# Performance work log

Measured on AMD Instinct MI355X. Metric: run time of the kernel, lower is better.

## Reference

```python
import jax, jax.numpy as jnp
import numpy as np

B, L, H, S = 8, 2048, 8, 128


def setup_inputs() -> dict:
    key = jax.random.key(0)
    k1, k2, k3 = jax.random.split(key, 3)
    x = jax.random.normal(k1, (B, L, S), dtype=jnp.float32)
    W = jax.random.normal(k2, (L, H), dtype=jnp.float32)          # per-head Toeplitz logits, W[j, h] fills diagonal -j
    A = jax.random.normal(k3, (H * S, H * S), dtype=jnp.float32)  # bilinear form for stage-2 attention
    return {"x": x, "W": W, "A": A}


def reference(x, W, A):
    Bb, Ll, Ss = x.shape
    Hh = W.shape[1]
    HS = Hh * Ss
    # Stage 1: causal Toeplitz softmax attention per head.
    # Original fills diagonal -j of W_h with W[j, h], masks strictly-upper with -inf, softmaxes rows.
    d = jnp.arange(Ll)[:, None] - jnp.arange(Ll)[None, :]          # (L, L), i - j
    logits = jnp.where(d[..., None] >= 0,
                       W[jnp.clip(d, 0, Ll - 1)],                  # (L, L, H), W[i-j, h] on valid band
                       -jnp.inf)
    P = jax.nn.softmax(logits, axis=1)                             # softmax over key axis j
    attn = jnp.einsum('ijh,bjs->bihs', P, x).reshape(Bb, Ll, HS)   # heads concatenated
    X1 = jnp.concatenate([attn, x], axis=-1)                       # (B, L, (H+1)*S)
    # Stage 2: single-query bilinear attention from last token over previous tokens.
    q = X1[:, -1, :HS]                                             # (B, HS)
    keys = X1[:, :-1, :HS]                                         # (B, L-1, HS)
    scores = jnp.einsum('bd,de,ble->bl', q, A, keys)               # (B, L-1)
    w2 = jax.nn.softmax(scores, axis=-1)
    # values are the raw-x slice X1[:, :-1, HS:] == x[:, :-1, :]
    out = jnp.einsum('bl,bls->bs', w2, x[:, :-1, :])               # (B, S)
    return out
```

## Files before the change

kernel.cpp:

```cpp
#include <hip/hip_runtime.h>

#define L 2048
#define H 8
#define S 128
#define B 8
#define HS 1024

__global__ __launch_bounds__(512) void kA_prep_qpart(const float* __restrict__ W,
                                                     const float* __restrict__ x,
                                                     float* __restrict__ Eb,
                                                     float* __restrict__ Zb,
                                                     float* __restrict__ partial_q,
                                                     unsigned* __restrict__ counters) {
  const int b = blockIdx.x, jc = blockIdx.y;
  const int t = threadIdx.x;
  if (b == 0 && jc == 0 && t < 8) counters[t] = 0u;

  __shared__ float ew[128][H];
  __shared__ float part[16][H][S];
  __shared__ float tot[512];

  const int base = jc * 128;
  const int dhi = L - 1 - base;
#pragma unroll
  for (int k = 0; k < 2; ++k) {
    const int idx = t + k * 512;
    const int i = idx >> 3, h = idx & 7;
    ew[i][h] = expf(W[(size_t)(dhi - i) * H + h]);
  }

  if (jc < H) {
    const int h = jc;
    const int d0 = t * 4;
    float e[4];
    float run = 0.f;
#pragma unroll
    for (int k = 0; k < 4; ++k) {
      float v = expf(W[(size_t)(d0 + k) * H + h]);
      e[k] = v; run += v;
    }
    tot[t] = run;
    __syncthreads();
    for (int off = 1; off < 512; off <<= 1) {
      float v = (t >= off) ? tot[t - off] : 0.f;
      __syncthreads();
      tot[t] += v;
      __syncthreads();
    }
    float c = (t == 0) ? 0.f : tot[t - 1];
    const size_t ebase = (size_t)(b * H + h) * L;
#pragma unroll
    for (int k = 0; k < 4; ++k) {
      c += e[k];
      Eb[ebase + d0 + k] = e[k];
      Zb[ebase + d0 + k] = c;
    }
  }
  __syncthreads();

  const int s4 = t & 31;
  const int r = t >> 5;
  const float4* __restrict__ x4 = (const float4*)(x + (size_t)b * L * S);
  float4 acc[H];
#pragma unroll
  for (int h = 0; h < H; ++h) acc[h] = make_float4(0.f, 0.f, 0.f, 0.f);
#pragma unroll
  for (int k = 0; k < 8; ++k) {
    const int ll = k * 16 + r;
    const int l = base + ll;
    const float4 xv = x4[(size_t)l * 32 + s4];
#pragma unroll
    for (int h = 0; h < H; ++h) {
      const float w = ew[ll][h];
      acc[h].x += w * xv.x; acc[h].y += w * xv.y;
      acc[h].z += w * xv.z; acc[h].w += w * xv.w;
    }
  }
#pragma unroll
  for (int h = 0; h < H; ++h) {
    part[r][h][s4 * 4 + 0] = acc[h].x;
    part[r][h][s4 * 4 + 1] = acc[h].y;
    part[r][h][s4 * 4 + 2] = acc[h].z;
    part[r][h][s4 * 4 + 3] = acc[h].w;
  }
  __syncthreads();
#pragma unroll
  for (int k = 0; k < 2; ++k) {
    const int idx = t + k * 512;
    const int h = idx >> 7, s = idx & 127;
    float sm = 0.f;
#pragma unroll
    for (int rr = 0; rr < 16; ++rr) sm += part[rr][h][s];
    partial_q[((size_t)b * 16 + jc) * HS + idx] = sm;
  }
}

__global__ __launch_bounds__(512) void kB_v(const float* __restrict__ partial_q,
                                            const float* __restrict__ Zb,
                                            const float* __restrict__ A,
                                            float* __restrict__ partial_v) {
  const int ebase = blockIdx.x * 128;
  const int dc = blockIdx.y;
  const int dbase = dc * 64;
  const int t = threadIdx.x;
  __shared__ float ql[8][64];
  __shared__ float p2[4][8][128];
  const float invZ = 1.f / Zb[(size_t)(dc >> 1) * L + (L - 1)];
  {
    const int bb = t >> 6, dl = t & 63;
    const float* __restrict__ pq = partial_q + ((size_t)bb * 16) * HS + dbase + dl;
    float a0 = 0.f, a1 = 0.f, a2 = 0.f, a3 = 0.f;
#pragma unroll
    for (int j4 = 0; j4 < 16; j4 += 4) {
      a0 += pq[(size_t)(j4 + 0) * HS];
      a1 += pq[(size_t)(j4 + 1) * HS];
      a2 += pq[(size_t)(j4 + 2) * HS];
      a3 += pq[(size_t)(j4 + 3) * HS];
    }
    ql[bb][dl] = ((a0 + a1) + (a2 + a3)) * invZ;
  }
  __syncthreads();
  const int el = t & 127, dg = t >> 7;
  const int e = ebase + el;
  const float* __restrict__ Ab = A + (size_t)(dbase + dg * 16) * HS + e;
  float acc[8] = {0.f, 0.f, 0.f, 0.f, 0.f, 0.f, 0.f, 0.f};
#pragma unroll 4
  for (int dd = 0; dd < 16; ++dd) {
    const float a = Ab[(size_t)dd * HS];
    const int d = dg * 16 + dd;
    acc[0] += ql[0][d] * a;
    acc[1] += ql[1][d] * a;
    acc[2] += ql[2][d] * a;
    acc[3] += ql[3][d] * a;
    acc[4] += ql[4][d] * a;
    acc[5] += ql[5][d] * a;
    acc[6] += ql[6][d] * a;
    acc[7] += ql[7][d] * a;
  }
#pragma unroll
  for (int bb = 0; bb < 8; ++bb) p2[dg][bb][el] = acc[bb];
  __syncthreads();
#pragma unroll
  for (int k = 0; k < 2; ++k) {
    const int idx = t + k * 512;
    const int bb = idx >> 7, el2 = idx & 127;
    partial_v[((size_t)bb * 16 + dc) * HS + ebase + el2] =
        (p2[0][bb][el2] + p2[1][bb][el2]) + (p2[2][bb][el2] + p2[3][bb][el2]);
  }
}

__global__ __launch_bounds__(512) void kC_u(const float* __restrict__ x,
                                            const float* __restrict__ partial_v,
                                            float* __restrict__ u_pad) {
  const int b = blockIdx.x, jc = blockIdx.y;
  const int t = threadIdx.x;
  __shared__ float vs[HS];
  __shared__ float up[4][H][128];
#pragma unroll
  for (int k = 0; k < 2; ++k) {
    const int i = t + k * 512;
    float a0 = 0.f, a1 = 0.f, a2 = 0.f, a3 = 0.f;
#pragma unroll
    for (int dcc = 0; dcc < 16; dcc += 4) {
      a0 += partial_v[((size_t)b * 16 + dcc + 0) * HS + i];
      a1 += partial_v[((size_t)b * 16 + dcc + 1) * HS + i];
      a2 += partial_v[((size_t)b * 16 + dcc + 2) * HS + i];
      a3 += partial_v[((size_t)b * 16 + dcc + 3) * HS + i];
    }
    vs[i] = (a0 + a1) + (a2 + a3);
  }
  __syncthreads();
  const int jl = t & 127, sq = t >> 7;
  const int j = jc * 128 + jl;
  const float4* __restrict__ xr = (const float4*)(x + ((size_t)b * L + j) * S) + sq * 8;
  float4 xv[8];
#pragma unroll
  for (int i = 0; i < 8; ++i) xv[i] = xr[i];
  float acc[H];
#pragma unroll
  for (int h = 0; h < H; ++h) {
    const float4* __restrict__ vv = (const float4*)(vs + h * S + sq * 32);
    float a = 0.f;
#pragma unroll
    for (int i = 0; i < 8; ++i) {
      const float4 w = vv[i];
      a += xv[i].x * w.x + xv[i].y * w.y + xv[i].z * w.z + xv[i].w * w.w;
    }
    acc[h] = a;
  }
#pragma unroll
  for (int h = 0; h < H; ++h) up[sq][h][jl] = acc[h];
  __syncthreads();
#pragma unroll
  for (int k = 0; k < 2; ++k) {
    const int idx = t + k * 512;
    const int h = idx >> 7, j2 = idx & 127;
    const float sv = (up[0][h][j2] + up[1][h][j2]) + (up[2][h][j2] + up[3][h][j2]);
    const size_t rowbase = (size_t)(b * H + h) * (2 * L);
    u_pad[rowbase + jc * 128 + j2] = 0.f;
    u_pad[rowbase + L + jc * 128 + j2] = sv;
  }
}

__global__ __launch_bounds__(512) void kDF_out(const float* __restrict__ x,
                                               const float* __restrict__ u_pad,
                                               const float* __restrict__ Eb,
                                               const float* __restrict__ Zb,
                                               float* __restrict__ scores,
                                               unsigned* __restrict__ counters,
                                               float* __restrict__ out) {
  const int b = blockIdx.x, lt = blockIdx.y;
  const int t = threadIdx.x;
  const int tsub = t & 31;
  const int h = (t >> 5) & 7;
  const int dh = t >> 8;
  const int l0 = lt * 128;
  const int Lb = l0 + tsub * 4;

  __shared__ float sred[2][H][128];
  __shared__ float ep[L];
  __shared__ float red[512];
  __shared__ float part[16][S];

  const float* __restrict__ ur = u_pad + (size_t)(b * H + h) * (2 * L) + L;
  const float4* __restrict__ Eh4 = (const float4*)(Eb + (size_t)(b * H + h) * L);
  float acc0 = 0.f, acc1 = 0.f, acc2 = 0.f, acc3 = 0.f;
  for (int chunk = dh; chunk <= lt; chunk += 2) {
    const int dbase = chunk * 128;
    float4 lo = *(const float4*)(ur + Lb - dbase - 4);
    float4 hi = *(const float4*)(ur + Lb - dbase);
#pragma unroll 4
    for (int dd = 0; dd < 128; dd += 4) {
      const int d0 = dbase + dd;
      float4 ev  = Eh4[d0 >> 2];
      float4 nlo = *(const float4*)(ur + Lb - d0 - 8);
      acc0 += ev.x * hi.x; acc1 += ev.x * hi.y; acc2 += ev.x * hi.z; acc3 += ev.x * hi.w;
      acc0 += ev.y * lo.w; acc1 += ev.y * hi.x; acc2 += ev.y * hi.y; acc3 += ev.y * hi.z;
      acc0 += ev.z * lo.z; acc1 += ev.z * lo.w; acc2 += ev.z * hi.x; acc3 += ev.z * hi.y;
      acc0 += ev.w * lo.y; acc1 += ev.w * lo.z; acc2 += ev.w * lo.w; acc3 += ev.w * hi.x;
      hi = lo; lo = nlo;
    }
  }
  const float4 zv = *(const float4*)&Zb[(size_t)(b * H + h) * L + Lb];
  sred[dh][h][tsub * 4 + 0] = acc0 / zv.x;
  sred[dh][h][tsub * 4 + 1] = acc1 / zv.y;
  sred[dh][h][tsub * 4 + 2] = acc2 / zv.z;
  sred[dh][h][tsub * 4 + 3] = acc3 / zv.w;
  __syncthreads();
  if (t < 128) {
    const int l = l0 + t;
    float sc = 0.f;
#pragma unroll
    for (int hh = 0; hh < H; ++hh) sc += sred[0][hh][t] + sred[1][hh][t];
    scores[(size_t)b * L + l] = (l == L - 1) ? -3.4e38f : sc;
  }

  __threadfence();
  __syncthreads();
  __shared__ unsigned lastFlag;
  if (t == 0)
    lastFlag = (atomicAdd(&counters[b], 1u) == 15u) ? 1u : 0u;
  __syncthreads();
  if (!lastFlag) return;

  const int l4 = t * 4;
  const float4 sv4 = *(const float4*)&scores[(size_t)b * L + l4];
  float mx = fmaxf(fmaxf(sv4.x, sv4.y), fmaxf(sv4.z, sv4.w));
  red[t] = mx;
  __syncthreads();
  for (int off = 256; off > 0; off >>= 1) {
    if (t < off) red[t] = fmaxf(red[t], red[t + off]);
    __syncthreads();
  }
  mx = red[0];
  __syncthreads();
  float e0 = expf(sv4.x - mx), e1 = expf(sv4.y - mx);
  float e2 = expf(sv4.z - mx), e3 = expf(sv4.w - mx);
  red[t] = (e0 + e1) + (e2 + e3);
  __syncthreads();
  for (int off = 256; off > 0; off >>= 1) {
    if (t < off) red[t] += red[t + off];
    __syncthreads();
  }
  const float inv = 1.f / red[0];
  ep[l4 + 0] = e0 * inv;
  ep[l4 + 1] = e1 * inv;
  ep[l4 + 2] = e2 * inv;
  ep[l4 + 3] = e3 * inv;
  __syncthreads();

  const int s4 = t & 31;
  const int r = t >> 5;
  const float4* __restrict__ x4 = (const float4*)(x + (size_t)b * L * S);
  float4 acc = make_float4(0.f, 0.f, 0.f, 0.f);
  for (int k = 0; k < 128; ++k) {
    const int l = k * 16 + r;
    const float w = ep[l];
    const float4 xv = x4[(size_t)l * 32 + s4];
    acc.x += w * xv.x; acc.y += w * xv.y; acc.z += w * xv.z; acc.w += w * xv.w;
  }
  part[r][s4 * 4 + 0] = acc.x;
  part[r][s4 * 4 + 1] = acc.y;
  part[r][s4 * 4 + 2] = acc.z;
  part[r][s4 * 4 + 3] = acc.w;
  __syncthreads();
  if (t < S) {
    float smv = 0.f;
#pragma unroll
    for (int rr = 0; rr < 16; ++rr) smv += part[rr][t];
    out[b * S + t] = smv;
  }
}

extern "C" void kernel_launch(void* const* d_in, const int* in_sizes, int n_in,
                              void* d_out, int out_size, void* d_ws, size_t ws_size,
                              hipStream_t stream) {
  const float* x = (const float*)d_in[0];
  const float* W = (const float*)d_in[1];
  const float* A = (const float*)d_in[2];
  float* out = (float*)d_out;

  float* ws        = (float*)d_ws;
  float* Eb        = ws;
  float* Zb        = Eb + (size_t)B * H * L;
  float* partial_q = Zb + (size_t)B * H * L;
  float* partial_v = partial_q + (size_t)B * 16 * HS;
  float* u_pad     = partial_v + (size_t)B * 16 * HS;
  float* scores    = u_pad + (size_t)B * H * 2 * L;
  unsigned* counters = (unsigned*)(scores + (size_t)B * L);

  kA_prep_qpart<<<dim3(B, 16), 512, 0, stream>>>(W, x, Eb, Zb, partial_q, counters);
  kB_v         <<<dim3(8, 16), 512, 0, stream>>>(partial_q, Zb, A, partial_v);
  kC_u         <<<dim3(B, 16), 512, 0, stream>>>(x, partial_v, u_pad);
  kDF_out      <<<dim3(B, 16), 512, 0, stream>>>(x, u_pad, Eb, Zb, scores, counters, out);
}
```

Before: 62.76 us.

## Split triangular Toeplitz convolution in kDF_out into balanced per-chunk blocks

Before, each kDF_out block walked a variable number of 128-wide d-chunks, so work grew with the l-tile and the blocks were unevenly loaded. Now 72 blocks per batch each handle one 256-wide chunk pair of the triangular iteration space and write partial scores. A two-level padded atomic counter picks the last block, which sums the partials before the softmax and weighted sum. This evens out the load and adds parallelism, at the cost of extra partial-score traffic and a more complex completion protocol.

```diff
diff --git a/kernel.cpp b/kernel.cpp
--- a/kernel.cpp
+++ b/kernel.cpp
@@ -14,7 +14,7 @@
                                                      unsigned* __restrict__ counters) {
   const int b = blockIdx.x, jc = blockIdx.y;
   const int t = threadIdx.x;
-  if (b == 0 && jc == 0 && t < 8) counters[t] = 0u;
+  if (b == 0 && jc == 0 && t < 72) counters[t * 16] = 0u;
 
   __shared__ float ew[128][H];
   __shared__ float part[16][H][S];
@@ -206,15 +206,20 @@
                                                const float* __restrict__ u_pad,
                                                const float* __restrict__ Eb,
                                                const float* __restrict__ Zb,
-                                               float* __restrict__ scores,
+                                               float* __restrict__ partial_s,
                                                unsigned* __restrict__ counters,
                                                float* __restrict__ out) {
-  const int b = blockIdx.x, lt = blockIdx.y;
+  const int b = blockIdx.x;
+  const int rr = blockIdx.y;
+  int lt = 0, c = 0;
+  while (c + (lt / 2 + 1) <= rr) { c += lt / 2 + 1; ++lt; }
+  const int dtt = rr - c;
+  const int l0 = lt * 128;
   const int t = threadIdx.x;
   const int tsub = t & 31;
   const int h = (t >> 5) & 7;
   const int dh = t >> 8;
-  const int l0 = lt * 128;
+  const int dbase = dtt * 256 + dh * 128;
   const int Lb = l0 + tsub * 4;
 
   __shared__ float sred[2][H][128];
@@ -222,11 +227,10 @@
   __shared__ float red[512];
   __shared__ float part[16][S];
 
-  const float* __restrict__ ur = u_pad + (size_t)(b * H + h) * (2 * L) + L;
-  const float4* __restrict__ Eh4 = (const float4*)(Eb + (size_t)(b * H + h) * L);
-  float acc0 = 0.f, acc1 = 0.f, acc2 = 0.f, acc3 = 0.f;
-  for (int chunk = dh; chunk <= lt; chunk += 2) {
-    const int dbase = chunk * 128;
+  {
+    const float* __restrict__ ur = u_pad + (size_t)(b * H + h) * (2 * L) + L;
+    const float4* __restrict__ Eh4 = (const float4*)(Eb + (size_t)(b * H + h) * L);
+    float acc0 = 0.f, acc1 = 0.f, acc2 = 0.f, acc3 = 0.f;
     float4 lo = *(const float4*)(ur + Lb - dbase - 4);
     float4 hi = *(const float4*)(ur + Lb - dbase);
 #pragma unroll 4
@@ -240,32 +244,46 @@
       acc0 += ev.w * lo.y; acc1 += ev.w * lo.z; acc2 += ev.w * lo.w; acc3 += ev.w * hi.x;
       hi = lo; lo = nlo;
     }
-  }
-  const float4 zv = *(const float4*)&Zb[(size_t)(b * H + h) * L + Lb];
-  sred[dh][h][tsub * 4 + 0] = acc0 / zv.x;
-  sred[dh][h][tsub * 4 + 1] = acc1 / zv.y;
-  sred[dh][h][tsub * 4 + 2] = acc2 / zv.z;
-  sred[dh][h][tsub * 4 + 3] = acc3 / zv.w;
-  __syncthreads();
-  if (t < 128) {
-    const int l = l0 + t;
-    float sc = 0.f;
-#pragma unroll
-    for (int hh = 0; hh < H; ++hh) sc += sred[0][hh][t] + sred[1][hh][t];
-    scores[(size_t)b * L + l] = (l == L - 1) ? -3.4e38f : sc;
+    const float4 zv = *(const float4*)&Zb[(size_t)(b * H + h) * L + Lb];
+    sred[dh][h][tsub * 4 + 0] = acc0 / zv.x;
+    sred[dh][h][tsub * 4 + 1] = acc1 / zv.y;
+    sred[dh][h][tsub * 4 + 2] = acc2 / zv.z;
+    sred[dh][h][tsub * 4 + 3] = acc3 / zv.w;
+    __syncthreads();
+    if (t < 128) {
+      float sc = 0.f;
+#pragma unroll
+      for (int hh = 0; hh < H; ++hh) sc += sred[0][hh][t] + sred[1][hh][t];
+      partial_s[((size_t)b * 8 + dtt) * L + l0 + t] = sc;
+    }
   }
 
   __threadfence();
   __syncthreads();
   __shared__ unsigned lastFlag;
-  if (t == 0)
-    lastFlag = (atomicAdd(&counters[b], 1u) == 15u) ? 1u : 0u;
+  if (t == 0) {
+    unsigned lf = 0u;
+    const int g = rr / 9;
+    const unsigned o1 = atomicAdd(&counters[(b * 8 + g) * 16], 1u);
+    if (o1 == 8u) {
+      const unsigned o2 = atomicAdd(&counters[(64 + b) * 16], 1u);
+      lf = (o2 == 7u) ? 1u : 0u;
+    }
+    lastFlag = lf;
+  }
   __syncthreads();
   if (!lastFlag) return;
+  __threadfence();
 
   const int l4 = t * 4;
-  const float4 sv4 = *(const float4*)&scores[(size_t)b * L + l4];
-  float mx = fmaxf(fmaxf(sv4.x, sv4.y), fmaxf(sv4.z, sv4.w));
+  const int ltq = t >> 6;
+  float sc[4] = {0.f, 0.f, 0.f, 0.f};
+  for (int d2 = 0; d2 <= ltq; ++d2) {
+    const float4 a = *(const float4*)(partial_s + ((size_t)b * 8 + d2) * L + l4);
+    sc[0] += a.x; sc[1] += a.y; sc[2] += a.z; sc[3] += a.w;
+  }
+  if (t == 511) sc[3] = -3.4e38f;
+  float mx = fmaxf(fmaxf(sc[0], sc[1]), fmaxf(sc[2], sc[3]));
   red[t] = mx;
   __syncthreads();
   for (int off = 256; off > 0; off >>= 1) {
@@ -274,8 +292,8 @@
   }
   mx = red[0];
   __syncthreads();
-  float e0 = expf(sv4.x - mx), e1 = expf(sv4.y - mx);
-  float e2 = expf(sv4.z - mx), e3 = expf(sv4.w - mx);
+  float e0 = expf(sc[0] - mx), e1 = expf(sc[1] - mx);
+  float e2 = expf(sc[2] - mx), e3 = expf(sc[3] - mx);
   red[t] = (e0 + e1) + (e2 + e3);
   __syncthreads();
   for (int off = 256; off > 0; off >>= 1) {
@@ -307,7 +325,7 @@
   if (t < S) {
     float smv = 0.f;
 #pragma unroll
-    for (int rr = 0; rr < 16; ++rr) smv += part[rr][t];
+    for (int rr2 = 0; rr2 < 16; ++rr2) smv += part[rr2][t];
     out[b * S + t] = smv;
   }
 }
@@ -326,11 +344,11 @@
   float* partial_q = Zb + (size_t)B * H * L;
   float* partial_v = partial_q + (size_t)B * 16 * HS;
   float* u_pad     = partial_v + (size_t)B * 16 * HS;
-  float* scores    = u_pad + (size_t)B * H * 2 * L;
-  unsigned* counters = (unsigned*)(scores + (size_t)B * L);
+  float* partial_s = u_pad + (size_t)B * H * 2 * L;
+  unsigned* counters = (unsigned*)(partial_s + (size_t)B * 8 * L);
 
   kA_prep_qpart<<<dim3(B, 16), 512, 0, stream>>>(W, x, Eb, Zb, partial_q, counters);
   kB_v         <<<dim3(8, 16), 512, 0, stream>>>(partial_q, Zb, A, partial_v);
   kC_u         <<<dim3(B, 16), 512, 0, stream>>>(x, partial_v, u_pad);
-  kDF_out      <<<dim3(B, 16), 512, 0, stream>>>(x, u_pad, Eb, Zb, scores, counters, out);
-}
+  kDF_out      <<<dim3(B, 72), 512, 0, stream>>>(x, u_pad, Eb, Zb, partial_s, counters, out);
+}
```

After: 107.8 us. 1.72x slower.
